# Optimization experiments

Measured on AMD Instinct MI355X. Metric: run time of the kernel, lower is better.

## Reference

```python
import jax, jax.numpy as jnp
import numpy as np

Q_MAX = 127.0  # symmetric int8 range

def setup_inputs() -> dict:
    key = jax.random.key(0)
    k1, k2, k3, k4 = jax.random.split(key, 4)
    B, S, K, N = 4, 2048, 4096, 4096
    inp = jax.random.normal(k1, (B, S, K), dtype=jnp.float32)
    # int8 weight in [-127, 127], stored via randint(0,255)-127 per spec
    qweight = (jax.random.randint(k2, (N, K), 0, 255) - 127).astype(jnp.int8)
    # per-out-channel weight dequant scales (small positive)
    wparams = (jax.random.uniform(k3, (N,), dtype=jnp.float32) * 0.02 + 0.001)
    bias = jax.random.normal(k4, (N,), dtype=jnp.float32) * 0.1
    return {"inp": inp, "qweight": qweight, "wparams": wparams, "bias": bias}

def reference(inp, qweight, wparams, bias):
    # inp: [B, S, K] float32; qweight: [N, K] int8; wparams: [N]; bias: [N]
    B, S, K = inp.shape
    x = inp.reshape(B * S, K)
    # qntz: per-row symmetric absmax quantization of the activation to int8
    a_scale = jnp.max(jnp.abs(x), axis=1, keepdims=True) / Q_MAX  # [M, 1]
    qinp = jnp.clip(jnp.round(x / a_scale), -Q_MAX, Q_MAX).astype(jnp.int8)  # [M, K]
    d = jax.lax.dot_general(qinp, qweight.T, (((1,), (0,)), ((), ())),
                            preferred_element_type=jnp.int32)  # [M, N]
    # dqntz: scale by per-row act scale and per-col weight scale, add bias
    out = d.astype(jnp.float32) * a_scale * wparams[None, :] + bias[None, :]
    return out.reshape(B, S, -1)
```

## Files before the change

kernel.cpp:

```cpp
#include <hip/hip_runtime.h>
#include <hip/hip_bf16.h>


using int32x4 = __attribute__((ext_vector_type(4))) int;

#define QMAXF 127.0f

__global__ __launch_bounds__(256) void repack_weights(
    const int* __restrict__ w, signed char* __restrict__ w8, int total)
{
    bool is32 = true;
#pragma unroll
    for (int i = 0; i < 16; ++i) {
        int v = w[i];
        is32 = is32 && (v >= -127 && v <= 127);
    }

    const int t = blockIdx.x * blockDim.x + threadIdx.x;
    const int nth = gridDim.x * blockDim.x;
    const int chunks = total / 16;

    if (is32) {
        for (int c = t; c < chunks; c += nth) {
            const int32x4* src = reinterpret_cast<const int32x4*>(w + (size_t)c * 16);
            int32x4 a0 = src[0], a1 = src[1], a2 = src[2], a3 = src[3];
            int32x4 o;
            o[0] = (a0[0] & 0xff) | ((a0[1] & 0xff) << 8) | ((a0[2] & 0xff) << 16) | ((a0[3] & 0xff) << 24);
            o[1] = (a1[0] & 0xff) | ((a1[1] & 0xff) << 8) | ((a1[2] & 0xff) << 16) | ((a1[3] & 0xff) << 24);
            o[2] = (a2[0] & 0xff) | ((a2[1] & 0xff) << 8) | ((a2[2] & 0xff) << 16) | ((a2[3] & 0xff) << 24);
            o[3] = (a3[0] & 0xff) | ((a3[1] & 0xff) << 8) | ((a3[2] & 0xff) << 16) | ((a3[3] & 0xff) << 24);
            reinterpret_cast<int32x4*>(w8)[c] = o;
        }
    } else {
        const int32x4* src = reinterpret_cast<const int32x4*>(w);
        int32x4* dst = reinterpret_cast<int32x4*>(w8);
        for (int c = t; c < chunks; c += nth) dst[c] = src[c];
    }
}

__global__ __launch_bounds__(256) void quant_rows(
    const float* __restrict__ x, signed char* __restrict__ q,
    float* __restrict__ scale, int K)
{
    const int row = blockIdx.x;
    const int t = threadIdx.x;
    const float4* xr = reinterpret_cast<const float4*>(x + (size_t)row * K);

    float4 v[4];
    float m = 0.f;
#pragma unroll
    for (int i = 0; i < 4; ++i) {
        v[i] = xr[t + i * 256];
        m = fmaxf(m, fmaxf(fmaxf(fabsf(v[i].x), fabsf(v[i].y)),
                           fmaxf(fabsf(v[i].z), fabsf(v[i].w))));
    }
#pragma unroll
    for (int off = 32; off >= 1; off >>= 1)
        m = fmaxf(m, __shfl_xor(m, off, 64));
    __shared__ float wmax[4];
    const int wave = t >> 6;
    if ((t & 63) == 0) wmax[wave] = m;
    __syncthreads();
    m = fmaxf(fmaxf(wmax[0], wmax[1]), fmaxf(wmax[2], wmax[3]));

    const float s   = m / QMAXF;
    const float inv = (m > 0.f) ? (QMAXF / m) : 0.f;
    if (t == 0) scale[row] = s;

    int* qr = reinterpret_cast<int*>(q + (size_t)row * K);
#pragma unroll
    for (int i = 0; i < 4; ++i) {
        const float* f = reinterpret_cast<const float*>(&v[i]);
        unsigned int packed = 0;
#pragma unroll
        for (int j = 0; j < 4; ++j) {
            int qi = __float2int_rn(f[j] * inv);
            qi = qi > 127 ? 127 : (qi < -127 ? -127 : qi);
            packed |= ((unsigned int)(qi & 0xff)) << (8 * j);
        }
        qr[t + i * 256] = (int)packed;
    }
}

#define BM 256
#define BN 256
#define BKB 64
#define NBUF 4

__device__ __forceinline__ void async_copy16(const void* g, void* lds) {
    __builtin_amdgcn_global_load_lds(
        (const __attribute__((address_space(1))) void*)g,
        (__attribute__((address_space(3))) void*)lds, 16, 0, 0);
}

#define BARF do {                                         \
    __builtin_amdgcn_sched_barrier(0);                    \
    asm volatile("" ::: "memory");                        \
    __builtin_amdgcn_s_barrier();                         \
    asm volatile("" ::: "memory");                        \
    __builtin_amdgcn_sched_barrier(0);                    \
} while (0)

#define LGKM0 asm volatile("s_waitcnt lgkmcnt(0)" ::: "memory")
#define VM4   asm volatile("s_waitcnt vmcnt(4)" ::: "memory")
#define VM2   asm volatile("s_waitcnt vmcnt(2)" ::: "memory")
#define VM0   asm volatile("s_waitcnt vmcnt(0)" ::: "memory")

__global__ __launch_bounds__(1024) void gemm_i8_dequant_16w(
    const signed char* __restrict__ A,
    const signed char* __restrict__ B,
    const float* __restrict__ a_scale,
    const float* __restrict__ wparams,
    const float* __restrict__ bias,
    float* __restrict__ out,
    int M, int N, int K)
{
    __shared__ __align__(16) signed char lds[NBUF * 32768];

    const int t    = threadIdx.x;
    const int lane = t & 63;
    const int wave = t >> 6;
    const int wr   = wave >> 2;
    const int wc   = wave & 3;

    const int nwg = gridDim.x;
    const int cpx = nwg >> 3;
    const int swz = (blockIdx.x & 7) * cpx + (blockIdx.x >> 3);
    const int nbx = N / BN;
    const int rowBase = (swz / nbx) * BM;
    const int colBase = (swz % nbx) * BN;

    const int r15 = lane & 15;
    const int ksl = lane >> 4;

    int32x4 acc[4][4] = {};
    const int NT = K / BKB;

    const signed char* gA = A + (size_t)(rowBase + wave * 16 + r15) * K + ksl * 16;
    const signed char* gB = B + (size_t)(colBase + wave * 16 + r15) * K + ksl * 16;

    auto stage = [&](int tile) {
        signed char* L = lds + (tile & (NBUF - 1)) * 32768;
        const size_t kt = (size_t)tile * BKB;
        async_copy16(gA + kt, L + wave * 1024);
        async_copy16(gB + kt, L + 16384 + wave * 1024);
    };

    auto computeTile = [&](int tile) {
        const signed char* Ab = lds + (tile & (NBUF - 1)) * 32768
                              + (wr * 4) * 1024 + lane * 16;
        const signed char* Bb = lds + (tile & (NBUF - 1)) * 32768 + 16384
                              + (wc * 4) * 1024 + lane * 16;
        int32x4 af[4], bf[4];
#pragma unroll
        for (int mm = 0; mm < 4; ++mm)
            af[mm] = *reinterpret_cast<const int32x4*>(Ab + mm * 1024);
#pragma unroll
        for (int nn = 0; nn < 4; ++nn)
            bf[nn] = *reinterpret_cast<const int32x4*>(Bb + nn * 1024);
        __builtin_amdgcn_s_setprio(1);
#pragma unroll
        for (int mm = 0; mm < 4; ++mm)
#pragma unroll
            for (int nn = 0; nn < 4; ++nn)
                acc[mm][nn] = __builtin_amdgcn_mfma_i32_16x16x64_i8(
                    af[mm], bf[nn], acc[mm][nn], 0, 0, 0);
        __builtin_amdgcn_s_setprio(0);
    };

    stage(0); stage(1); stage(2);
    VM4;
    BARF;

    for (int tt = 0; tt < NT - 3; ++tt) {
        stage(tt + 3);
        computeTile(tt);
        VM4;
        LGKM0;
        BARF;
    }
    computeTile(NT - 3);
    VM2; LGKM0; BARF;
    computeTile(NT - 2);
    VM0; LGKM0; BARF;
    computeTile(NT - 1);

#pragma unroll
    for (int mm = 0; mm < 4; ++mm) {
        const int rb = rowBase + wr * 64 + mm * 16 + ksl * 4;
        float asc[4];
#pragma unroll
        for (int r = 0; r < 4; ++r) asc[r] = a_scale[rb + r];
#pragma unroll
        for (int nn = 0; nn < 4; ++nn) {
            const int col = colBase + wc * 64 + nn * 16 + r15;
            const float wp = wparams[col];
            const float bs = bias[col];
#pragma unroll
            for (int r = 0; r < 4; ++r) {
                out[(size_t)(rb + r) * N + col] =
                    (float)acc[mm][nn][r] * asc[r] * wp + bs;
            }
        }
    }
}

extern "C" void kernel_launch(void* const* d_in, const int* in_sizes, int n_in,
                              void* d_out, int out_size, void* d_ws, size_t ws_size,
                              hipStream_t stream) {
    const float* inp     = (const float*)d_in[0];
    const int*   qw_raw  = (const int*)d_in[1];
    const float* wparams = (const float*)d_in[2];
    const float* bias    = (const float*)d_in[3];
    float*       out     = (float*)d_out;

    const int N = in_sizes[2];
    const int K = in_sizes[1] / N;
    const int M = in_sizes[0] / K;

    signed char* qinp    = (signed char*)d_ws;
    float*       a_scale = (float*)((char*)d_ws + (size_t)M * K);
    size_t off_w8 = (size_t)M * K + (((size_t)M * sizeof(float) + 255) & ~(size_t)255);
    signed char* w8      = (signed char*)((char*)d_ws + off_w8);

    repack_weights<<<2048, 256, 0, stream>>>(qw_raw, w8, N * K);
    quant_rows<<<M, 256, 0, stream>>>(inp, qinp, a_scale, K);

    const int nwg = (M / BM) * (N / BN);
    gemm_i8_dequant_16w<<<nwg, 1024, 0, stream>>>(
        qinp, w8, a_scale, wparams, bias, out, M, N, K);
}
```

Measured before the change: 204.7 us.

## Switch GEMM to double-buffered 128-deep K tiles with two-phase fragment loads

The GEMM K-tile grows from 64 to 128 bytes and the four-stage LDS ring becomes two 64KB buffers. Each iteration issues the next tile's async copies, then runs two half-tile phases (load fragments, MFMA) separated by barriers, and waits for vmcnt(0) at the end. This halves the number of loop iterations and barriers per K and interleaves LDS reads with MFMA work. The cost is only one tile of prefetch lookahead, where there were three, so global latency is less hidden, and there are extra barriers inside each iteration.

```diff
diff --git a/kernel.cpp b/kernel.cpp
--- a/kernel.cpp
+++ b/kernel.cpp
@@ -84,8 +84,9 @@
 
 #define BM 256
 #define BN 256
-#define BKB 64
-#define NBUF 4
+#define BKB 128
+#define NBUF 2
+#define BUFSZ 65536
 
 __device__ __forceinline__ void async_copy16(const void* g, void* lds) {
     __builtin_amdgcn_global_load_lds(
@@ -102,11 +103,9 @@
 } while (0)
 
 #define LGKM0 asm volatile("s_waitcnt lgkmcnt(0)" ::: "memory")
-#define VM4   asm volatile("s_waitcnt vmcnt(4)" ::: "memory")
-#define VM2   asm volatile("s_waitcnt vmcnt(2)" ::: "memory")
 #define VM0   asm volatile("s_waitcnt vmcnt(0)" ::: "memory")
 
-__global__ __launch_bounds__(1024) void gemm_i8_dequant_16w(
+__global__ __launch_bounds__(1024) void gemm_i8_dequant_ph16(
     const signed char* __restrict__ A,
     const signed char* __restrict__ B,
     const float* __restrict__ a_scale,
@@ -115,7 +114,7 @@
     float* __restrict__ out,
     int M, int N, int K)
 {
-    __shared__ __align__(16) signed char lds[NBUF * 32768];
+    __shared__ __align__(16) signed char lds[NBUF * BUFSZ];
 
     const int t    = threadIdx.x;
     const int lane = t & 63;
@@ -136,54 +135,73 @@
     int32x4 acc[4][4] = {};
     const int NT = K / BKB;
 
-    const signed char* gA = A + (size_t)(rowBase + wave * 16 + r15) * K + ksl * 16;
-    const signed char* gB = B + (size_t)(colBase + wave * 16 + r15) * K + ksl * 16;
+    const int rg0 = wave >> 1, sl0 = wave & 1;
+    const signed char* gA0 = A + (size_t)(rowBase + rg0 * 16 + r15) * K
+                               + sl0 * 64 + ksl * 16;
+    const signed char* gA1 = A + (size_t)(rowBase + (8 + rg0) * 16 + r15) * K
+                               + sl0 * 64 + ksl * 16;
+    const signed char* gB0 = B + (size_t)(colBase + rg0 * 16 + r15) * K
+                               + sl0 * 64 + ksl * 16;
+    const signed char* gB1 = B + (size_t)(colBase + (8 + rg0) * 16 + r15) * K
+                               + sl0 * 64 + ksl * 16;
+    const int fi0 = wave, fi1 = 16 + wave;
 
     auto stage = [&](int tile) {
-        signed char* L = lds + (tile & (NBUF - 1)) * 32768;
+        signed char* L = lds + (tile & 1) * BUFSZ;
         const size_t kt = (size_t)tile * BKB;
-        async_copy16(gA + kt, L + wave * 1024);
-        async_copy16(gB + kt, L + 16384 + wave * 1024);
+        async_copy16(gA0 + kt, L + fi0 * 1024);
+        async_copy16(gA1 + kt, L + fi1 * 1024);
+        async_copy16(gB0 + kt, L + 32768 + fi0 * 1024);
+        async_copy16(gB1 + kt, L + 32768 + fi1 * 1024);
     };
 
-    auto computeTile = [&](int tile) {
-        const signed char* Ab = lds + (tile & (NBUF - 1)) * 32768
-                              + (wr * 4) * 1024 + lane * 16;
-        const signed char* Bb = lds + (tile & (NBUF - 1)) * 32768 + 16384
-                              + (wc * 4) * 1024 + lane * 16;
-        int32x4 af[4], bf[4];
+    auto ldFragsSl = [&](int tile, int sl, int32x4 (&fa)[4], int32x4 (&fb)[4]) {
+        const signed char* base = lds + (tile & 1) * BUFSZ + lane * 16;
 #pragma unroll
         for (int mm = 0; mm < 4; ++mm)
-            af[mm] = *reinterpret_cast<const int32x4*>(Ab + mm * 1024);
+            fa[mm] = *reinterpret_cast<const int32x4*>(
+                base + ((wr * 4 + mm) * 2 + sl) * 1024);
 #pragma unroll
         for (int nn = 0; nn < 4; ++nn)
-            bf[nn] = *reinterpret_cast<const int32x4*>(Bb + nn * 1024);
+            fb[nn] = *reinterpret_cast<const int32x4*>(
+                base + 32768 + ((wc * 4 + nn) * 2 + sl) * 1024);
+    };
+
+    auto mfma16 = [&](const int32x4 (&fa)[4], const int32x4 (&fb)[4]) {
         __builtin_amdgcn_s_setprio(1);
 #pragma unroll
         for (int mm = 0; mm < 4; ++mm)
 #pragma unroll
             for (int nn = 0; nn < 4; ++nn)
                 acc[mm][nn] = __builtin_amdgcn_mfma_i32_16x16x64_i8(
-                    af[mm], bf[nn], acc[mm][nn], 0, 0, 0);
+                    fa[mm], fb[nn], acc[mm][nn], 0, 0, 0);
         __builtin_amdgcn_s_setprio(0);
     };
 
-    stage(0); stage(1); stage(2);
-    VM4;
+    int32x4 af[4], bf[4];
+
+    stage(0);
+    VM0;
     BARF;
 
-    for (int tt = 0; tt < NT - 3; ++tt) {
-        stage(tt + 3);
-        computeTile(tt);
-        VM4;
+    for (int tt = 0; tt < NT - 1; ++tt) {
+        ldFragsSl(tt, 0, af, bf);
+        stage(tt + 1);
+        BARF; LGKM0;
+        mfma16(af, bf);
+        BARF;
+        ldFragsSl(tt, 1, af, bf);
         LGKM0;
+        mfma16(af, bf);
+        VM0;
         BARF;
     }
-    computeTile(NT - 3);
-    VM2; LGKM0; BARF;
-    computeTile(NT - 2);
-    VM0; LGKM0; BARF;
-    computeTile(NT - 1);
+    ldFragsSl(NT - 1, 0, af, bf);
+    LGKM0;
+    mfma16(af, bf);
+    ldFragsSl(NT - 1, 1, af, bf);
+    LGKM0;
+    mfma16(af, bf);
 
 #pragma unroll
     for (int mm = 0; mm < 4; ++mm) {
@@ -227,6 +245,6 @@
     quant_rows<<<M, 256, 0, stream>>>(inp, qinp, a_scale, K);
 
     const int nwg = (M / BM) * (N / BN);
-    gemm_i8_dequant_16w<<<nwg, 1024, 0, stream>>>(
+    gemm_i8_dequant_ph16<<<nwg, 1024, 0, stream>>>(
         qinp, w8, a_scale, wparams, bias, out, M, N, K);
 }
```

Result: slower. 216.2 us (+5.6%).
